# Optimization experiments

Measured on AMD Instinct MI355X. Metric: run time of the kernel, lower is better.

The kernel has to match this reference:

```python
import math
import jax, jax.numpy as jnp
import numpy as np

H = 12
D_MODEL = 768
D_K = D_MODEL // H
B, S = 2, 2048


def setup_inputs() -> dict:
    key = jax.random.key(0)
    ks = jax.random.split(key, 12)
    sc = 0.02
    inp = {
        "query": jax.random.normal(ks[0], (B, S, D_MODEL), jnp.float32),
        "key": jax.random.normal(ks[1], (B, S, D_MODEL), jnp.float32),
        "value": jax.random.normal(ks[2], (B, S, D_MODEL), jnp.float32),
        # causal mask [B, S, S]: 1 where attendable
        "mask": jnp.broadcast_to(jnp.tril(jnp.ones((S, S), jnp.int32)), (B, S, S)),
        "Wq": sc * jax.random.normal(ks[3], (D_MODEL, D_MODEL), jnp.float32),
        "bq": jnp.zeros((D_MODEL,), jnp.float32),
        "Wk": sc * jax.random.normal(ks[4], (D_MODEL, D_MODEL), jnp.float32),
        "bk": jnp.zeros((D_MODEL,), jnp.float32),
        "Wv": sc * jax.random.normal(ks[5], (D_MODEL, D_MODEL), jnp.float32),
        "bv": jnp.zeros((D_MODEL,), jnp.float32),
        "Wo": sc * jax.random.normal(ks[6], (D_MODEL, D_MODEL), jnp.float32),
        "bo": jnp.zeros((D_MODEL,), jnp.float32),
    }
    return inp


def reference(query, key, value, mask, Wq, bq, Wk, bk, Wv, bv, Wo, bo):
    b, s, _ = query.shape
    # linear projections (torch Linear: x @ W.T + b), split into heads
    def proj(x, W, bias):
        return (x @ W.T + bias).reshape(b, s, H, D_K).transpose(0, 2, 1, 3)  # [B,H,S,Dk]

    q = proj(query, Wq, bq)
    k = proj(key, Wk, bk)
    v = proj(value, Wv, bv)

    scores = jnp.einsum("bhqd,bhkd->bhqk", q, k) / math.sqrt(D_K)  # [B,H,S,S]
    # exponential time-decay bias over key positions 1..S, shape [1,1,1,S]
    time = jnp.exp(-jnp.arange(1, s + 1, dtype=scores.dtype))[None, None, None, :]
    scores = jnp.where(mask[:, None, :, :] == 0, jnp.asarray(-1e9, scores.dtype), scores)
    p_attn = jax.nn.softmax(scores - time, axis=-1)
    x = jnp.einsum("bhqk,bhkd->bhqd", p_attn, v)  # [B,H,S,Dk]
    x = x.transpose(0, 2, 1, 3).reshape(b, s, H * D_K)
    return x @ Wo.T + bo
```

## Files before the change

### kernel.cpp

```cpp
#include <hip/hip_runtime.h>
#include <hip/hip_bf16.h>
#include <math.h>

typedef __bf16 bf16;
typedef __attribute__((ext_vector_type(8))) __bf16 bf16x8;
typedef __attribute__((ext_vector_type(4))) __bf16 bf16x4;
typedef __attribute__((ext_vector_type(4))) float floatx4;

#define NH 12
#define DK 64
#define DM 768
#define NB 2
#define SEQ 2048
#define MTOT (NB * SEQ)
#define WELEM (DM * DM)
#define XELEM (MTOT * DM)

#define QSCALE 0.1803368801111832f
#define LOG2E 1.4426950408889634f

static __device__ __forceinline__ bf16x8 load8(const bf16* p) {
    return *(const bf16x8*)p;
}
static __device__ __forceinline__ float4 ld4(const float* p) {
    return *(const float4*)p;
}
static __device__ __forceinline__ bf16x8 cvt8(const float4 a, const float4 b) {
    bf16x8 r;
    r[0] = (bf16)a.x; r[1] = (bf16)a.y; r[2] = (bf16)a.z; r[3] = (bf16)a.w;
    r[4] = (bf16)b.x; r[5] = (bf16)b.y; r[6] = (bf16)b.z; r[7] = (bf16)b.w;
    return r;
}
static __device__ __forceinline__ float fast_exp2(float x) {
#if __has_builtin(__builtin_amdgcn_exp2f)
    return __builtin_amdgcn_exp2f(x);
#else
    return __expf(x * 0.6931471805599453f);
#endif
}
static __device__ __forceinline__ void async16(const bf16* g, bf16* l) {
    __builtin_amdgcn_global_load_lds((const __attribute__((address_space(1))) void*)g,
                                     (__attribute__((address_space(3))) void*)l,
                                     16, 0, 0);
}

__global__ __launch_bounds__(256) void cvt_kernel(
    const float* __restrict__ wq, const float* __restrict__ wk,
    const float* __restrict__ wv, const float* __restrict__ wo,
    const float* __restrict__ xq, const float* __restrict__ xk, const float* __restrict__ xv,
    bf16* __restrict__ Wb, bf16* __restrict__ Wob,
    bf16* __restrict__ Xqb, bf16* __restrict__ Xkb, bf16* __restrict__ Xvb) {
    const int g = blockIdx.x * 256 + threadIdx.x;
    const int PW = WELEM / 8;
    const int PX = XELEM / 8;
    if (g < 4 * PW) {
        const int wi = g / PW;
        const int rem = g - wi * PW;
        const int n = rem / 96;
        const int t = rem - n * 96;
        const int s = t >> 3;
        const int j = t & 7;
        const float* src = (wi == 0) ? wq : (wi == 1) ? wk : (wi == 2) ? wv : wo;
        bf16* dst = (wi < 3) ? (Wb + (size_t)wi * WELEM) : Wob;
        const float* p = src + (size_t)n * DM + s * 64 + j * 8;
        *(bf16x8*)(dst + (size_t)n * DM + s * 64 + ((j ^ (n & 7)) * 8)) = cvt8(ld4(p), ld4(p + 4));
    } else {
        const int gx = g - 4 * PW;
        const int xi = gx / PX;
        const int rem = gx - xi * PX;
        const int m = rem / 96;
        const int t = rem - m * 96;
        const int s = t >> 3;
        const int j = t & 7;
        const float* src = (xi == 0) ? xq : (xi == 1) ? xk : xv;
        bf16* dst = (xi == 0) ? Xqb : (xi == 1) ? Xkb : Xvb;
        const float* p = src + (size_t)m * DM + s * 64 + j * 8;
        *(bf16x8*)(dst + (size_t)m * DM + s * 64 + ((j ^ (m & 7)) * 8)) = cvt8(ld4(p), ld4(p + 4));
    }
}

__global__ __launch_bounds__(256, 3) void qkv_kernel(
    const bf16* __restrict__ Xqb, const bf16* __restrict__ Xkb, const bf16* __restrict__ Xvb,
    const bf16* __restrict__ Wb,
    const float* __restrict__ bq, const float* __restrict__ bk, const float* __restrict__ bv,
    bf16* __restrict__ Oq, bf16* __restrict__ Ok, bf16* __restrict__ Ov) {
    __shared__ __align__(16) bf16 SM[2 * 64 * 64 + 2 * 128 * 64];
    bf16* As0 = SM;
    bf16* Bs0 = SM + 8192;

    const int tid = threadIdx.x;
    const int id = blockIdx.x;
    const int xcd = id & 7;
    const int sl = id >> 3;
    const int z = sl / 48;
    const int r = sl % 48;
    const int m0 = (xcd * 8 + r / 6) * 64;
    const int n0 = (r % 6) * 128;

    const bf16* X = (z == 0) ? Xqb : (z == 1) ? Xkb : Xvb;
    const bf16* W = Wb + (size_t)z * WELEM;
    const float* bias = (z == 0) ? bq : (z == 1) ? bk : bv;
    bf16* out = (z == 0) ? Oq : (z == 1) ? Ok : Ov;

    const int wv = tid >> 6;
    const int wm = wv >> 1, wn = wv & 1;
    const int lane = tid & 63;
    const int ln = lane & 15;
    const int kq = lane >> 4;
    const int drow = lane >> 3;
    const int dcol = (lane & 7) * 8;

    floatx4 acc[2][4];
#pragma unroll
    for (int i = 0; i < 2; i++)
#pragma unroll
        for (int j = 0; j < 4; j++) acc[i][j] = (floatx4){0.f, 0.f, 0.f, 0.f};

#pragma unroll
    for (int it = 0; it < 2; it++)
        async16(X + (size_t)(m0 + wv * 16 + it * 8 + drow) * DM + dcol,
                As0 + (wv * 16 + it * 8) * 64);
#pragma unroll
    for (int it = 0; it < 4; it++)
        async16(W + (size_t)(n0 + wv * 32 + it * 8 + drow) * DM + dcol,
                Bs0 + (wv * 32 + it * 8) * 64);

    for (int k = 0; k < 12; k++) {
        __syncthreads();
        const bf16* Ap = As0 + (k & 1) * 4096;
        const bf16* Bp = Bs0 + (k & 1) * 8192;
        if (k < 11) {
            const int kc = (k + 1) * 64;
            bf16* An = As0 + ((k + 1) & 1) * 4096;
            bf16* Bn = Bs0 + ((k + 1) & 1) * 8192;
#pragma unroll
            for (int it = 0; it < 2; it++)
                async16(X + (size_t)(m0 + wv * 16 + it * 8 + drow) * DM + kc + dcol,
                        An + (wv * 16 + it * 8) * 64);
#pragma unroll
            for (int it = 0; it < 4; it++)
                async16(W + (size_t)(n0 + wv * 32 + it * 8 + drow) * DM + kc + dcol,
                        Bn + (wv * 32 + it * 8) * 64);
        }
#pragma unroll
        for (int ks = 0; ks < 2; ks++) {
            const int jb = (ks * 4 + kq) ^ (ln & 7);
            bf16x8 af[2], bfm[4];
#pragma unroll
            for (int mt = 0; mt < 2; mt++)
                af[mt] = *(const bf16x8*)&Ap[(wm * 32 + mt * 16 + ln) * 64 + jb * 8];
#pragma unroll
            for (int nt = 0; nt < 4; nt++)
                bfm[nt] = *(const bf16x8*)&Bp[(wn * 64 + nt * 16 + ln) * 64 + jb * 8];
#pragma unroll
            for (int mt = 0; mt < 2; mt++)
#pragma unroll
                for (int nt = 0; nt < 4; nt++)
                    acc[mt][nt] = __builtin_amdgcn_mfma_f32_16x16x32_bf16(af[mt], bfm[nt], acc[mt][nt], 0, 0, 0);
        }
    }

    float bv4[4];
#pragma unroll
    for (int nt = 0; nt < 4; nt++) bv4[nt] = bias[n0 + wn * 64 + nt * 16 + ln];

    if (z < 2) {
        const float qs = (z == 0) ? QSCALE : 1.0f;
        __syncthreads();
        bf16 (*E)[136] = (bf16(*)[136])SM;
#pragma unroll
        for (int mt = 0; mt < 2; mt++)
#pragma unroll
            for (int nt = 0; nt < 4; nt++)
#pragma unroll
                for (int r2 = 0; r2 < 4; r2++)
                    E[wm * 32 + mt * 16 + kq * 4 + r2][wn * 64 + nt * 16 + ln] =
                        (bf16)((acc[mt][nt][r2] + bv4[nt]) * qs);
        __syncthreads();
        const int row = tid >> 2;
        const int cb = (tid & 3) * 32;
        const int m = m0 + row;
        const int b = m >> 11;
        const int s = m & (SEQ - 1);
        const int h = (n0 + cb) >> 6;
        const int d = (n0 + cb) & 63;
        bf16* op = &out[((size_t)(b * NH + h) * SEQ + s) * DK + d];
#pragma unroll
        for (int q2 = 0; q2 < 4; q2++)
            *(bf16x8*)(op + q2 * 8) = *(bf16x8*)&E[row][cb + q2 * 8];
    } else {
        __syncthreads();
        bf16 (*E)[72] = (bf16(*)[72])SM;
#pragma unroll
        for (int nt = 0; nt < 4; nt++)
#pragma unroll
            for (int mt = 0; mt < 2; mt++) {
                bf16x4 v;
#pragma unroll
                for (int r2 = 0; r2 < 4; r2++) v[r2] = (bf16)(acc[mt][nt][r2] + bv4[nt]);
                *(bf16x4*)&E[wn * 64 + nt * 16 + ln][wm * 32 + mt * 16 + kq * 4] = v;
            }
        __syncthreads();
        const int row = tid >> 1;
        const int sc = (tid & 1) * 32;
        const int b = m0 >> 11;
        const int s0 = m0 & (SEQ - 1);
        const int h = (n0 >> 6) + (row >> 6);
        const int d = row & 63;
        bf16* op = &out[(size_t)(b * NH + h) * DK * SEQ + (size_t)d * SEQ + s0 + sc];
#pragma unroll
        for (int q2 = 0; q2 < 4; q2++)
            *(bf16x8*)(op + q2 * 8) = *(bf16x8*)&E[row][sc + q2 * 8];
    }
}


#define QK_BODY(FIRSTC)                                                        \
    _Pragma("unroll")                                                          \
    for (int ks = 0; ks < 8; ks++) {                                           \
        const bf16x8 a0 = load8(Kp + (size_t)(k0 + (ks >> 1) * 32 + (ks & 1) * 4) * DK); \
        const bf16x8 a1 = load8(Kp + (size_t)(k0 + (ks >> 1) * 32 + (ks & 1) * 4) * DK + 32); \
        floatx4 t = (floatx4){0.f, 0.f, 0.f, 0.f};                             \
        t = __builtin_amdgcn_mfma_f32_16x16x32_bf16(a0, qa0, t, 0, 0, 0);      \
        t = __builtin_amdgcn_mfma_f32_16x16x32_bf16(a1, qa1, t, 0, 0, 0);      \
        const int kbase = k0 + (ks >> 1) * 32 + (ks & 1) * 4 + kq * 8;         \
        _Pragma("unroll")                                                      \
        for (int r = 0; r < 4; r++) {                                          \
            const int kg = kbase + r;                                          \
            float sv = t[r];                                                   \
            if (FIRSTC) sv -= __expf(-(float)(kg + 1)) * LOG2E;                \
            float pf = fast_exp2(sv);                                          \
            if (lastc && kg > qgl) pf = 0.f;                                   \
            lsum += pf;                                                        \
            pa[ks >> 1][(ks & 1) * 4 + r] = (bf16)pf;                          \
        }                                                                      \
    }

__global__ __launch_bounds__(256) void attn_kernel(const bf16* __restrict__ Q,
                                                   const bf16* __restrict__ K,
                                                   const bf16* __restrict__ Vt,
                                                   bf16* __restrict__ Xout) {
    __shared__ bf16 Vs[2][64][136];

    const int tid = threadIdx.x;
    const int wv = tid >> 6;
    const int lane = tid & 63;
    const int ln = lane & 15;
    const int kq = lane >> 4;
    const int vrow = tid >> 2;
    const int vcol = (tid & 3) * 32;

    const int bidx = blockIdx.x;
    const int rk = (bidx < 256 || bidx >= 512) ? bidx : 767 - bidx;
    const int x = 31 - (rk / 24);
    const int bh = rk % 24;

    const int q0 = x * 64;
    const int qbase = q0 + wv * 16;
    const int nch = (x >> 1) + 1;

    const bf16* Qb = Q + (size_t)bh * SEQ * DK;
    const bf16* Kb = K + (size_t)bh * SEQ * DK;
    const bf16* Vb = Vt + (size_t)bh * SEQ * DK;

    const bf16x8 qa0 = load8(&Qb[(size_t)(qbase + ln) * DK + kq * 8]);
    const bf16x8 qa1 = load8(&Qb[(size_t)(qbase + ln) * DK + 32 + kq * 8]);

    const int pln = ((ln >> 2) << 3) | (ln & 3);
    const bf16* Kp = Kb + (size_t)pln * DK + kq * 8;

    bf16x8 vx[4];
#pragma unroll
    for (int q = 0; q < 4; q++) vx[q] = load8(&Vb[(size_t)vrow * SEQ + vcol + q * 8]);

    float lsum = 0.f;
    floatx4 Oacc[4];
#pragma unroll
    for (int nt = 0; nt < 4; nt++) Oacc[nt] = (floatx4){0.f, 0.f, 0.f, 0.f};

    const int qgl = qbase + ln;

    for (int c = 0; c < nch; c++) {
        const int k0 = c * 128;
        const bool lastc = (c == nch - 1);

        bf16x8 pa[4];
        if (c == 0) {
            QK_BODY(true)
        } else {
            QK_BODY(false)
        }

#pragma unroll
        for (int q = 0; q < 4; q++) *(bf16x8*)&Vs[c & 1][vrow][vcol + q * 8] = vx[q];

        if (c + 1 < nch) {
            const int kn = k0 + 128;
#pragma unroll
            for (int q = 0; q < 4; q++)
                vx[q] = load8(&Vb[(size_t)vrow * SEQ + kn + vcol + q * 8]);
        }

        __syncthreads();

        __builtin_amdgcn_s_setprio(1);
#pragma unroll
        for (int nt = 0; nt < 4; nt++) {
#pragma unroll
            for (int seg = 0; seg < 4; seg++) {
                const bf16x8 vb = *(bf16x8*)&Vs[c & 1][nt * 16 + ln][seg * 32 + kq * 8];
                Oacc[nt] = __builtin_amdgcn_mfma_f32_16x16x32_bf16(pa[seg], vb, Oacc[nt], 0, 0, 0);
            }
        }
        __builtin_amdgcn_s_setprio(0);
    }

    lsum += __shfl_xor(lsum, 16, 64);
    lsum += __shfl_xor(lsum, 32, 64);
    float rl[4];
#pragma unroll
    for (int r = 0; r < 4; r++) rl[r] = 1.f / __shfl(lsum, kq * 4 + r, 64);

    __syncthreads();
    bf16 (*E)[72] = (bf16(*)[72])Vs;
    const int erow = tid >> 2;
    const int ecb = (tid & 3) * 16;
#pragma unroll
    for (int nt = 0; nt < 4; nt++) {
#pragma unroll
        for (int r = 0; r < 4; r++)
            E[wv * 16 + kq * 4 + r][nt * 16 + ln] = (bf16)(Oacc[nt][r] * rl[r]);
    }
    __syncthreads();
    const int b = bh / NH;
    const int h = bh - b * NH;
    const int q = q0 + erow;
    const int j0 = (tid & 3) * 2;
    const int key = erow & 7;
    bf16* rowp = &Xout[((size_t)(b * SEQ + q)) * DM + h * DK];
    *(bf16x8*)(rowp + ((j0 ^ key) * 8)) = *(bf16x8*)&E[erow][ecb];
    *(bf16x8*)(rowp + (((j0 + 1) ^ key) * 8)) = *(bf16x8*)&E[erow][ecb + 8];
}

__global__ __launch_bounds__(256, 3) void outproj_kernel(const bf16* __restrict__ X,
                                                         const bf16* __restrict__ W,
                                                         const float* __restrict__ bias,
                                                         float* __restrict__ out) {
    __shared__ __align__(16) bf16 SM[2 * 64 * 64 + 2 * 128 * 64];
    bf16* As0 = SM;
    bf16* Bs0 = SM + 8192;

    const int tid = threadIdx.x;
    const int id = blockIdx.x;
    const int xcd = id & 7;
    const int sl = id >> 3;
    const int m0 = (xcd * 8 + sl / 6) * 64;
    const int n0 = (sl % 6) * 128;

    const int wv = tid >> 6;
    const int wm = wv >> 1, wn = wv & 1;
    const int lane = tid & 63;
    const int ln = lane & 15;
    const int kq = lane >> 4;
    const int drow = lane >> 3;
    const int dcol = (lane & 7) * 8;

    floatx4 acc[2][4];
#pragma unroll
    for (int i = 0; i < 2; i++)
#pragma unroll
        for (int j = 0; j < 4; j++) acc[i][j] = (floatx4){0.f, 0.f, 0.f, 0.f};

#pragma unroll
    for (int it = 0; it < 2; it++)
        async16(X + (size_t)(m0 + wv * 16 + it * 8 + drow) * DM + dcol,
                As0 + (wv * 16 + it * 8) * 64);
#pragma unroll
    for (int it = 0; it < 4; it++)
        async16(W + (size_t)(n0 + wv * 32 + it * 8 + drow) * DM + dcol,
                Bs0 + (wv * 32 + it * 8) * 64);

    for (int k = 0; k < 12; k++) {
        __syncthreads();
        const bf16* Ap = As0 + (k & 1) * 4096;
        const bf16* Bp = Bs0 + (k & 1) * 8192;
        if (k < 11) {
            const int kc = (k + 1) * 64;
            bf16* An = As0 + ((k + 1) & 1) * 4096;
            bf16* Bn = Bs0 + ((k + 1) & 1) * 8192;
#pragma unroll
            for (int it = 0; it < 2; it++)
                async16(X + (size_t)(m0 + wv * 16 + it * 8 + drow) * DM + kc + dcol,
                        An + (wv * 16 + it * 8) * 64);
#pragma unroll
            for (int it = 0; it < 4; it++)
                async16(W + (size_t)(n0 + wv * 32 + it * 8 + drow) * DM + kc + dcol,
                        Bn + (wv * 32 + it * 8) * 64);
        }
#pragma unroll
        for (int ks = 0; ks < 2; ks++) {
            const int jb = (ks * 4 + kq) ^ (ln & 7);
            bf16x8 af[2], bfm[4];
#pragma unroll
            for (int mt = 0; mt < 2; mt++)
                af[mt] = *(const bf16x8*)&Ap[(wm * 32 + mt * 16 + ln) * 64 + jb * 8];
#pragma unroll
            for (int nt = 0; nt < 4; nt++)
                bfm[nt] = *(const bf16x8*)&Bp[(wn * 64 + nt * 16 + ln) * 64 + jb * 8];
#pragma unroll
            for (int mt = 0; mt < 2; mt++)
#pragma unroll
                for (int nt = 0; nt < 4; nt++)
                    acc[mt][nt] = __builtin_amdgcn_mfma_f32_16x16x32_bf16(af[mt], bfm[nt], acc[mt][nt], 0, 0, 0);
        }
    }

#pragma unroll
    for (int nt = 0; nt < 4; nt++) {
        const int n = n0 + wn * 64 + nt * 16 + ln;
        const float bval = bias[n];
#pragma unroll
        for (int mt = 0; mt < 2; mt++)
#pragma unroll
            for (int r2 = 0; r2 < 4; r2++) {
                const int m = m0 + wm * 32 + mt * 16 + kq * 4 + r2;
                out[(size_t)m * DM + n] = acc[mt][nt][r2] + bval;
            }
    }
}

extern "C" void kernel_launch(void* const* d_in, const int* in_sizes, int n_in,
                              void* d_out, int out_size, void* d_ws, size_t ws_size,
                              hipStream_t stream) {
    const float* query = (const float*)d_in[0];
    const float* key   = (const float*)d_in[1];
    const float* value = (const float*)d_in[2];
    const float* Wq = (const float*)d_in[4];
    const float* bq = (const float*)d_in[5];
    const float* Wk = (const float*)d_in[6];
    const float* bk = (const float*)d_in[7];
    const float* Wv = (const float*)d_in[8];
    const float* bv = (const float*)d_in[9];
    const float* Wo = (const float*)d_in[10];
    const float* bo = (const float*)d_in[11];
    float* out = (float*)d_out;

    bf16* Qws  = (bf16*)d_ws;
    bf16* Kws  = Qws + XELEM;
    bf16* Vtws = Kws + XELEM;
    bf16* Xws  = Vtws + XELEM;
    bf16* Wob  = Xws + XELEM;
    bf16* Xvb  = Wob + WELEM;

    bf16* Wb  = (bf16*)out;
    bf16* Xkb = (bf16*)out + 3 * WELEM;

    bf16* Xqb = Xws;

    const int ncvt = (4 * (WELEM / 8) + 3 * (XELEM / 8)) / 256;
    cvt_kernel<<<ncvt, 256, 0, stream>>>(Wq, Wk, Wv, Wo, query, key, value,
                                         Wb, Wob, Xqb, Xkb, Xvb);

    qkv_kernel<<<1152, 256, 0, stream>>>(Xqb, Xkb, Xvb, Wb, bq, bk, bv,
                                         Qws, Kws, Vtws);

    attn_kernel<<<768, 256, 0, stream>>>(Qws, Kws, Vtws, Xws);

    outproj_kernel<<<384, 256, 0, stream>>>(Xws, Wob, bo, out);
}
```

Baseline: 224.4 us.

## Restructure attention to 128-row query tiles with 32x32 MFMA and async K/V staging

The attention kernel now gives each workgroup 128 query rows (32 per wave) instead of 64. It uses 32x32x16 bf16 MFMA for both QK and PV in place of 16x16x32, and stages swizzled K and V tiles into double-buffered LDS with global_load_lds async copies. Before, K was read straight from global memory and V was copied through registers. The goal is more K/V reuse per load, fewer loads overall and overlap of the next tile's fetch with compute. In exchange the grid halves to 384 blocks, which may lower occupancy and worsen load balance, and each lane holds larger accumulators, raising register pressure.

```diff
diff --git a/kernel.cpp b/kernel.cpp
--- a/kernel.cpp
+++ b/kernel.cpp
@@ -6,6 +6,7 @@
 typedef __attribute__((ext_vector_type(8))) __bf16 bf16x8;
 typedef __attribute__((ext_vector_type(4))) __bf16 bf16x4;
 typedef __attribute__((ext_vector_type(4))) float floatx4;
+typedef __attribute__((ext_vector_type(16))) float floatx16;
 
 #define NH 12
 #define DK 64
@@ -37,6 +38,12 @@
 #else
     return __expf(x * 0.6931471805599453f);
 #endif
+}
+static __device__ __forceinline__ floatx16 zero16() {
+    floatx16 z;
+#pragma unroll
+    for (int i = 0; i < 16; i++) z[i] = 0.f;
+    return z;
 }
 static __device__ __forceinline__ void async16(const bf16* g, bf16* l) {
     __builtin_amdgcn_global_load_lds((const __attribute__((address_space(1))) void*)g,
@@ -215,131 +222,151 @@
 }
 
 
-#define QK_BODY(FIRSTC)                                                        \
-    _Pragma("unroll")                                                          \
-    for (int ks = 0; ks < 8; ks++) {                                           \
-        const bf16x8 a0 = load8(Kp + (size_t)(k0 + (ks >> 1) * 32 + (ks & 1) * 4) * DK); \
-        const bf16x8 a1 = load8(Kp + (size_t)(k0 + (ks >> 1) * 32 + (ks & 1) * 4) * DK + 32); \
-        floatx4 t = (floatx4){0.f, 0.f, 0.f, 0.f};                             \
-        t = __builtin_amdgcn_mfma_f32_16x16x32_bf16(a0, qa0, t, 0, 0, 0);      \
-        t = __builtin_amdgcn_mfma_f32_16x16x32_bf16(a1, qa1, t, 0, 0, 0);      \
-        const int kbase = k0 + (ks >> 1) * 32 + (ks & 1) * 4 + kq * 8;         \
-        _Pragma("unroll")                                                      \
-        for (int r = 0; r < 4; r++) {                                          \
-            const int kg = kbase + r;                                          \
-            float sv = t[r];                                                   \
-            if (FIRSTC) sv -= __expf(-(float)(kg + 1)) * LOG2E;                \
-            float pf = fast_exp2(sv);                                          \
-            if (lastc && kg > qgl) pf = 0.f;                                   \
-            lsum += pf;                                                        \
-            pa[ks >> 1][(ks & 1) * 4 + r] = (bf16)pf;                          \
-        }                                                                      \
+#define PERMK(r) (((r) & ~12) | (((r) & 4) << 1) | (((r) & 8) >> 1))
+#define VSWZ(g, d) (((g) & 8) | (((g) & 7) ^ ((d) & 7)))
+
+#define STAGE(kc, bfsel)                                                            \
+    {                                                                               \
+        bf16* kb_ = SM + (bfsel) * 16384;                                           \
+        bf16* vb_ = kb_ + 8192;                                                     \
+        const int kk0 = (kc) * 128;                                                 \
+        _Pragma("unroll")                                                           \
+        for (int it = 0; it < 4; it++) {                                            \
+            const int sk = wv * 4 + it;                                             \
+            const int rK = sk * 8 + (lane >> 3);                                    \
+            const int jbK = lane & 7;                                               \
+            async16(Kb + (size_t)(kk0 + PERMK(rK)) * DK + ((jbK ^ (rK & 7)) * 8),   \
+                    kb_ + sk * 512);                                                \
+            const int dV = sk * 4 + (lane >> 4);                                    \
+            const int jbV = lane & 15;                                              \
+            async16(Vb + (size_t)dV * SEQ + kk0 + (VSWZ(jbV, dV) * 8),              \
+                    vb_ + sk * 512);                                                \
+        }                                                                           \
+    }
+
+#define CHUNK_BODY(FIRSTC)                                                          \
+    _Pragma("unroll")                                                               \
+    for (int c2 = 0; c2 < 4; c2++) {                                                \
+        const int rowk = c2 * 32 + ln32;                                            \
+        const bf16* krow = Kc + rowk * 64;                                          \
+        const int rs = rowk & 7;                                                    \
+        const bf16x8 a0 = *(const bf16x8*)&krow[((0 + hi) ^ rs) * 8];               \
+        const bf16x8 a1 = *(const bf16x8*)&krow[((2 + hi) ^ rs) * 8];               \
+        const bf16x8 a2 = *(const bf16x8*)&krow[((4 + hi) ^ rs) * 8];               \
+        const bf16x8 a3 = *(const bf16x8*)&krow[((6 + hi) ^ rs) * 8];               \
+        floatx16 tA = zero16(), tB = zero16();                                      \
+        __builtin_amdgcn_s_setprio(1);                                              \
+        tA = __builtin_amdgcn_mfma_f32_32x32x16_bf16(a0, qb0, tA, 0, 0, 0);         \
+        tA = __builtin_amdgcn_mfma_f32_32x32x16_bf16(a1, qb1, tA, 0, 0, 0);         \
+        tB = __builtin_amdgcn_mfma_f32_32x32x16_bf16(a2, qb2, tB, 0, 0, 0);         \
+        tB = __builtin_amdgcn_mfma_f32_32x32x16_bf16(a3, qb3, tB, 0, 0, 0);         \
+        __builtin_amdgcn_s_setprio(0);                                              \
+        bf16x8 pa0, pa1;                                                            \
+        _Pragma("unroll")                                                           \
+        for (int r = 0; r < 16; r++) {                                              \
+            const int kg = k0 + c2 * 32 + ((r >> 3) << 4) + (hi << 3) + (r & 7);    \
+            float sv = tA[r] + tB[r];                                               \
+            if (FIRSTC) sv -= __expf(-(float)(kg + 1)) * LOG2E;                     \
+            float pf = fast_exp2(sv);                                               \
+            if (lastc && kg > qgl) pf = 0.f;                                        \
+            lsum += pf;                                                             \
+            if (r < 8) pa0[r] = (bf16)pf; else pa1[r & 7] = (bf16)pf;               \
+        }                                                                           \
+        __builtin_amdgcn_s_setprio(1);                                              \
+        {                                                                           \
+            const bf16* v0 = Vc + ln32 * 128;                                       \
+            const bf16* v1 = Vc + (32 + ln32) * 128;                                \
+            const int ds = ln32 & 7;                                                \
+            bf16x8 vb;                                                              \
+            vb = *(const bf16x8*)&v0[VSWZ(c2 * 4 + hi, ds) * 8];                    \
+            Oacc0 = __builtin_amdgcn_mfma_f32_32x32x16_bf16(pa0, vb, Oacc0, 0, 0, 0); \
+            vb = *(const bf16x8*)&v0[VSWZ(c2 * 4 + 2 + hi, ds) * 8];                \
+            Oacc0 = __builtin_amdgcn_mfma_f32_32x32x16_bf16(pa1, vb, Oacc0, 0, 0, 0); \
+            vb = *(const bf16x8*)&v1[VSWZ(c2 * 4 + hi, ds) * 8];                    \
+            Oacc1 = __builtin_amdgcn_mfma_f32_32x32x16_bf16(pa0, vb, Oacc1, 0, 0, 0); \
+            vb = *(const bf16x8*)&v1[VSWZ(c2 * 4 + 2 + hi, ds) * 8];                \
+            Oacc1 = __builtin_amdgcn_mfma_f32_32x32x16_bf16(pa1, vb, Oacc1, 0, 0, 0); \
+        }                                                                           \
+        __builtin_amdgcn_s_setprio(0);                                              \
     }
 
 __global__ __launch_bounds__(256) void attn_kernel(const bf16* __restrict__ Q,
                                                    const bf16* __restrict__ K,
                                                    const bf16* __restrict__ Vt,
                                                    bf16* __restrict__ Xout) {
-    __shared__ bf16 Vs[2][64][136];
+    __shared__ __align__(16) bf16 SM[2 * 16384];
 
     const int tid = threadIdx.x;
     const int wv = tid >> 6;
     const int lane = tid & 63;
-    const int ln = lane & 15;
-    const int kq = lane >> 4;
-    const int vrow = tid >> 2;
-    const int vcol = (tid & 3) * 32;
-
-    const int bidx = blockIdx.x;
-    const int rk = (bidx < 256 || bidx >= 512) ? bidx : 767 - bidx;
-    const int x = 31 - (rk / 24);
-    const int bh = rk % 24;
-
-    const int q0 = x * 64;
-    const int qbase = q0 + wv * 16;
-    const int nch = (x >> 1) + 1;
+    const int ln32 = lane & 31;
+    const int hi = lane >> 5;
+
+    const int b0 = blockIdx.x;
+    const int t = (b0 < 192) ? (15 - b0 / 24) : ((b0 - 192) / 24);
+    const int bh = b0 % 24;
+
+    const int q0 = t * 128;
+    const int nch = t + 1;
 
     const bf16* Qb = Q + (size_t)bh * SEQ * DK;
     const bf16* Kb = K + (size_t)bh * SEQ * DK;
     const bf16* Vb = Vt + (size_t)bh * SEQ * DK;
 
-    const bf16x8 qa0 = load8(&Qb[(size_t)(qbase + ln) * DK + kq * 8]);
-    const bf16x8 qa1 = load8(&Qb[(size_t)(qbase + ln) * DK + 32 + kq * 8]);
-
-    const int pln = ((ln >> 2) << 3) | (ln & 3);
-    const bf16* Kp = Kb + (size_t)pln * DK + kq * 8;
-
-    bf16x8 vx[4];
-#pragma unroll
-    for (int q = 0; q < 4; q++) vx[q] = load8(&Vb[(size_t)vrow * SEQ + vcol + q * 8]);
+    const int qrow = q0 + wv * 32 + ln32;
+    const int qgl = qrow;
+
+    const bf16x8 qb0 = load8(Qb + (size_t)qrow * DK + 0 + hi * 8);
+    const bf16x8 qb1 = load8(Qb + (size_t)qrow * DK + 16 + hi * 8);
+    const bf16x8 qb2 = load8(Qb + (size_t)qrow * DK + 32 + hi * 8);
+    const bf16x8 qb3 = load8(Qb + (size_t)qrow * DK + 48 + hi * 8);
 
     float lsum = 0.f;
-    floatx4 Oacc[4];
-#pragma unroll
-    for (int nt = 0; nt < 4; nt++) Oacc[nt] = (floatx4){0.f, 0.f, 0.f, 0.f};
-
-    const int qgl = qbase + ln;
+    floatx16 Oacc0 = zero16(), Oacc1 = zero16();
+
+    STAGE(0, 0)
 
     for (int c = 0; c < nch; c++) {
         const int k0 = c * 128;
+        asm volatile("s_waitcnt vmcnt(0)" ::: "memory");
+        __syncthreads();
+        if (c + 1 < nch) STAGE(c + 1, (c + 1) & 1)
+        const bf16* Kc = SM + (c & 1) * 16384;
+        const bf16* Vc = Kc + 8192;
         const bool lastc = (c == nch - 1);
-
-        bf16x8 pa[4];
         if (c == 0) {
-            QK_BODY(true)
+            CHUNK_BODY(true)
         } else {
-            QK_BODY(false)
+            CHUNK_BODY(false)
         }
-
-#pragma unroll
-        for (int q = 0; q < 4; q++) *(bf16x8*)&Vs[c & 1][vrow][vcol + q * 8] = vx[q];
-
-        if (c + 1 < nch) {
-            const int kn = k0 + 128;
-#pragma unroll
-            for (int q = 0; q < 4; q++)
-                vx[q] = load8(&Vb[(size_t)vrow * SEQ + kn + vcol + q * 8]);
-        }
-
-        __syncthreads();
-
-        __builtin_amdgcn_s_setprio(1);
-#pragma unroll
-        for (int nt = 0; nt < 4; nt++) {
-#pragma unroll
-            for (int seg = 0; seg < 4; seg++) {
-                const bf16x8 vb = *(bf16x8*)&Vs[c & 1][nt * 16 + ln][seg * 32 + kq * 8];
-                Oacc[nt] = __builtin_amdgcn_mfma_f32_16x16x32_bf16(pa[seg], vb, Oacc[nt], 0, 0, 0);
-            }
-        }
-        __builtin_amdgcn_s_setprio(0);
-    }
-
-    lsum += __shfl_xor(lsum, 16, 64);
+    }
+
     lsum += __shfl_xor(lsum, 32, 64);
-    float rl[4];
-#pragma unroll
-    for (int r = 0; r < 4; r++) rl[r] = 1.f / __shfl(lsum, kq * 4 + r, 64);
+    const float inv = 1.f / lsum;
 
     __syncthreads();
-    bf16 (*E)[72] = (bf16(*)[72])Vs;
-    const int erow = tid >> 2;
-    const int ecb = (tid & 3) * 16;
-#pragma unroll
-    for (int nt = 0; nt < 4; nt++) {
-#pragma unroll
-        for (int r = 0; r < 4; r++)
-            E[wv * 16 + kq * 4 + r][nt * 16 + ln] = (bf16)(Oacc[nt][r] * rl[r]);
+    bf16 (*E)[72] = (bf16(*)[72])SM;
+#pragma unroll
+    for (int r = 0; r < 16; r++) {
+        const int rq = (r & 3) + ((r >> 2) << 3) + (hi << 2);
+        const float rv = __shfl(inv, rq, 64);
+        E[wv * 32 + rq][ln32] = (bf16)(Oacc0[r] * rv);
+        E[wv * 32 + rq][32 + ln32] = (bf16)(Oacc1[r] * rv);
     }
     __syncthreads();
+
     const int b = bh / NH;
     const int h = bh - b * NH;
-    const int q = q0 + erow;
-    const int j0 = (tid & 3) * 2;
-    const int key = erow & 7;
+    const int row = tid >> 1;
+    const int colh = (tid & 1) * 32;
+    const int q = q0 + row;
+    const int key = row & 7;
     bf16* rowp = &Xout[((size_t)(b * SEQ + q)) * DM + h * DK];
-    *(bf16x8*)(rowp + ((j0 ^ key) * 8)) = *(bf16x8*)&E[erow][ecb];
-    *(bf16x8*)(rowp + (((j0 + 1) ^ key) * 8)) = *(bf16x8*)&E[erow][ecb + 8];
+#pragma unroll
+    for (int s2 = 0; s2 < 4; s2++) {
+        const int jb = (tid & 1) * 4 + s2;
+        *(bf16x8*)(rowp + ((jb ^ key) * 8)) = *(bf16x8*)&E[row][colh + s2 * 8];
+    }
 }
 
 __global__ __launch_bounds__(256, 3) void outproj_kernel(const bf16* __restrict__ X,
@@ -464,7 +491,7 @@
     qkv_kernel<<<1152, 256, 0, stream>>>(Xqb, Xkb, Xvb, Wb, bq, bk, bv,
                                          Qws, Kws, Vtws);
 
-    attn_kernel<<<768, 256, 0, stream>>>(Qws, Kws, Vtws, Xws);
+    attn_kernel<<<384, 256, 0, stream>>>(Qws, Kws, Vtws, Xws);
 
     outproj_kernel<<<384, 256, 0, stream>>>(Xws, Wob, bo, out);
 }
```

After: 207.0 us. 7.8% less time.
